# Kernel tuning notes

Measured on AMD Instinct MI355X. Metric: run time of the kernel, lower is better.

Reference implementation:

```python
import jax, jax.numpy as jnp
import numpy as np

N_NODES = 50000
N_EDGES = 800000
NFEAT, NHID, NCLASS = 256, 64, 2


def _deg_norm(idx, n_nodes, dtype):
    deg = jax.ops.segment_sum(jnp.ones(idx.shape[0], dtype=dtype), idx, num_segments=n_nodes)
    return jax.lax.rsqrt(jnp.maximum(deg, 1.0))


def gcn_layer(x, W, b, src, dst, n_nodes):
    # DGL GraphConv, norm='both': h = D_in^{-1/2} * Agg( D_out^{-1/2} * x ) W + b
    # weight applied before aggregation (in_feats >= out_feats path); math-equivalent.
    norm_src = _deg_norm(src, n_nodes, x.dtype)  # out-degree norm of source nodes
    norm_dst = _deg_norm(dst, n_nodes, x.dtype)  # in-degree norm of dest nodes
    h = (x * norm_src[:, None]) @ W              # [N, out]
    agg = jax.ops.segment_sum(h[src], dst, num_segments=n_nodes)  # gather + scatter-add
    return agg * norm_dst[:, None] + b


def setup_inputs() -> dict:
    key = jax.random.key(0)
    k1, k2, k3, k4, k5, k6, k7 = jax.random.split(key, 7)
    x = jax.random.normal(k1, (N_NODES, NFEAT), dtype=jnp.float32)
    src = jax.random.randint(k2, (N_EDGES,), 0, N_NODES, dtype=jnp.int64)
    dst = jax.random.randint(k3, (N_EDGES,), 0, N_NODES, dtype=jnp.int64)
    # Glorot-style init like DGL GraphConv
    W1 = jax.random.normal(k4, (NFEAT, NHID), dtype=jnp.float32) * (2.0 / (NFEAT + NHID)) ** 0.5
    b1 = jnp.zeros((NHID,), dtype=jnp.float32)
    W2 = jax.random.normal(k5, (NHID, NCLASS), dtype=jnp.float32) * (2.0 / (NHID + NCLASS)) ** 0.5
    b2 = jnp.zeros((NCLASS,), dtype=jnp.float32)
    return {"x": x, "src": src, "dst": dst, "W1": W1, "b1": b1, "W2": W2, "b2": b2}


def reference(x, src, dst, W1, b1, W2, b2):
    h = jax.nn.relu(gcn_layer(x, W1, b1, src, dst, N_NODES))
    # dropout=False -> p=0, no-op
    logits = gcn_layer(h, W2, b2, src, dst, N_NODES)
    return jax.nn.log_softmax(logits, axis=1)
```

## Files before the change

kernel.cpp:

```cpp
#include <hip/hip_runtime.h>
#include <math.h>

#define N_NODES 50000
#define N_EDGES 800000
#define NFEAT 256
#define NHID 64
#define NCLASS 2

#define DB 64
#define NDB 782
#define BCAP 1536
#define EPB 2048
#define NB_EDGE ((N_EDGES + EPB - 1) / EPB)

#define OFF_CURD 0
#define OFF_CURS 800
#define OFF_RB   1600
#define OFF_DEG  51600
#define OFF_NDST 101600
#define OFF_NSRC 151600
#define OFF_W1T  201600
#define OFF_DPK  209792
#define OFF_SV6  1410944
#define OFF_CSR  1711232
#define OFF_HB   2912384
#define OFF_H2   4512384

typedef __attribute__((ext_vector_type(8))) short bf16x8;
typedef __attribute__((ext_vector_type(8))) short short8;
typedef __attribute__((ext_vector_type(4))) float f32x4;

static __device__ __forceinline__ unsigned short f2bf(float f) {
    union { float f; unsigned int u; } v; v.f = f;
    return (unsigned short)((v.u + 0x8000u) >> 16);
}
static __device__ __forceinline__ unsigned int pk2bf(float f0, float f1) {
    union { float f; unsigned int u; } a, b; a.f = f0; b.f = f1;
    return __builtin_amdgcn_perm(b.u + 0x8000u, a.u + 0x8000u, 0x07060302u);
}
static __device__ __forceinline__ float bflo(unsigned int u) {
    union { unsigned int x; float f; } v; v.x = u << 16; return v.f;
}
static __device__ __forceinline__ float bfhi(unsigned int u) {
    union { unsigned int x; float f; } v; v.x = u & 0xffff0000u; return v.f;
}

__global__ __launch_bounds__(256) void w1cvt_kernel(const float* __restrict__ W1,
                                                    unsigned short* __restrict__ w1t) {
    int idx = blockIdx.x * 256 + threadIdx.x;
    if (idx < NFEAT * NHID) {
        int k = idx >> 6, n = idx & 63;
        w1t[n * NFEAT + k] = f2bf(W1[idx]);
    }
}

__global__ __launch_bounds__(256) void bscatter_kernel(const int* __restrict__ src,
                                                       const int* __restrict__ dst,
                                                       int* __restrict__ cur_d,
                                                       int* __restrict__ cur_s,
                                                       int* __restrict__ dpk,
                                                       unsigned char* __restrict__ sv6) {
    __shared__ int hd[NDB], bd[NDB], cd[NDB], hs[NDB], bs[NDB], cs[NDB];
    int t = threadIdx.x;
    for (int i = t; i < NDB; i += 256) { hd[i] = 0; cd[i] = 0; hs[i] = 0; cs[i] = 0; }
    __syncthreads();
    int base = blockIdx.x * EPB;
    int ls[8], ld[8];
#pragma unroll
    for (int i = 0; i < 8; ++i) {
        int e = base + t + i * 256;
        ls[i] = (e < N_EDGES) ? src[e] : -1;
        ld[i] = (e < N_EDGES) ? dst[e] : -1;
        if (ld[i] >= 0) {
            atomicAdd(&hd[ld[i] >> 6], 1);
            atomicAdd(&hs[ls[i] >> 6], 1);
        }
    }
    __syncthreads();
    for (int i = t; i < NDB; i += 256) {
        if (hd[i]) bd[i] = atomicAdd(&cur_d[i], hd[i]);
        if (hs[i]) bs[i] = atomicAdd(&cur_s[i], hs[i]);
    }
    __syncthreads();
#pragma unroll
    for (int i = 0; i < 8; ++i) {
        if (ld[i] >= 0) {
            int bin = ld[i] >> 6;
            int pos = bd[bin] + atomicAdd(&cd[bin], 1);
            dpk[bin * BCAP + pos] = (ls[i] << 6) | (ld[i] & 63);
            int sbin = ls[i] >> 6;
            int spos = bs[sbin] + atomicAdd(&cs[sbin], 1);
            sv6[sbin * BCAP + spos] = (unsigned char)(ls[i] & 63);
        }
    }
}

__global__ __launch_bounds__(256) void dfin_kernel(const int* __restrict__ cur_d,
                                                   const int* __restrict__ dpk,
                                                   int* __restrict__ row_beg,
                                                   int* __restrict__ degv,
                                                   float* __restrict__ norm_dst,
                                                   int* __restrict__ csr) {
    __shared__ int ebuf[BCAP];
    __shared__ int hist4[4 * 64], hist[64], seg[64], cur[64];
    int b = blockIdx.x, t = threadIdx.x;
    int cnt = cur_d[b];
    int base = b * BCAP;
    if (t < 64) { hist[t] = 0; cur[t] = 0; }
    hist4[t] = 0;
    for (int j = t; j < cnt; j += 256) ebuf[j] = dpk[base + j];
    __syncthreads();
    int sub = (t & 3) * 64;
    for (int j = t; j < cnt; j += 256) atomicAdd(&hist4[sub + (ebuf[j] & 63)], 1);
    __syncthreads();
    if (t < 64) {
        int v = hist4[t] + hist4[64 + t] + hist4[128 + t] + hist4[192 + t];
        hist[t] = v;
        seg[t] = v;
    }
    __syncthreads();
#pragma unroll
    for (int off = 1; off < 64; off <<= 1) {
        int xv = 0;
        if (t < 64 && t >= off) xv = seg[t - off];
        __syncthreads();
        if (t < 64) seg[t] += xv;
        __syncthreads();
    }
    if (t < 64) {
        int v = hist[t];
        int excl = seg[t] - v;
        int gid = b * 64 + t;
        if (gid < N_NODES) {
            row_beg[gid] = base + excl;
            degv[gid] = v;
            norm_dst[gid] = rsqrtf(fmaxf((float)v, 1.0f));
        }
        seg[t] = excl;
    }
    __syncthreads();
    for (int j = t; j < cnt; j += 256) {
        int p = ebuf[j];
        int dlow = p & 63;
        int pos = base + seg[dlow] + atomicAdd(&cur[dlow], 1);
        csr[pos] = ((unsigned)p) >> 6;
    }
}

__global__ __launch_bounds__(256) void sfin_kernel(const int* __restrict__ cur_s,
                                                   const unsigned char* __restrict__ sv6,
                                                   float* __restrict__ norm_src) {
    __shared__ int hist4[4 * 64];
    int b = blockIdx.x, t = threadIdx.x;
    hist4[t] = 0;
    __syncthreads();
    int cnt = cur_s[b];
    int base = b * BCAP;
    int sub = (t & 3) * 64;
    for (int j = t; j < cnt; j += 256) atomicAdd(&hist4[sub + sv6[base + j]], 1);
    __syncthreads();
    if (t < 64) {
        int gid = b * 64 + t;
        if (gid < N_NODES) {
            int v = hist4[t] + hist4[64 + t] + hist4[128 + t] + hist4[192 + t];
            norm_src[gid] = rsqrtf(fmaxf((float)v, 1.0f));
        }
    }
}

#define LDA 264
__global__ __launch_bounds__(256) void gemm1_kernel(const float* __restrict__ x,
                                                    const unsigned short* __restrict__ w1t,
                                                    const float* __restrict__ norm_src,
                                                    unsigned short* __restrict__ hb) {
    __shared__ unsigned short As[64][LDA];
    __shared__ unsigned short Bs[64][LDA];
    const int t = threadIdx.x;
    const int row0 = blockIdx.x * 64;
#pragma unroll
    for (int i = 0; i < 16; ++i) {
        int f = i * 256 + t;
        int r = f >> 6;
        int c4 = (f & 63) * 4;
        int grow = row0 + r;
        float4 av = make_float4(0.f, 0.f, 0.f, 0.f);
        if (grow < N_NODES) av = *(const float4*)(&x[(size_t)grow * NFEAT + c4]);
        uint2 o;
        o.x = pk2bf(av.x, av.y);
        o.y = pk2bf(av.z, av.w);
        *(uint2*)(&As[r][c4]) = o;
    }
#pragma unroll
    for (int i = 0; i < 8; ++i) {
        int c = i * 256 + t;
        int n = c >> 5;
        int k8 = (c & 31) * 8;
        *(short8*)(&Bs[n][k8]) = *(const short8*)(&w1t[n * NFEAT + k8]);
    }
    __syncthreads();
    const int w = t >> 6;
    const int l = t & 63;
    const int m = l & 15;
    const int kq = (l >> 4) * 8;
    f32x4 acc[4] = {{0.f, 0.f, 0.f, 0.f}, {0.f, 0.f, 0.f, 0.f},
                    {0.f, 0.f, 0.f, 0.f}, {0.f, 0.f, 0.f, 0.f}};
#pragma unroll
    for (int c8 = 0; c8 < 8; ++c8) {
        int k0 = c8 * 32 + kq;
        bf16x8 a = *(const bf16x8*)(&As[w * 16 + m][k0]);
#pragma unroll
        for (int ct = 0; ct < 4; ++ct) {
            bf16x8 b = *(const bf16x8*)(&Bs[ct * 16 + m][k0]);
            acc[ct] = __builtin_amdgcn_mfma_f32_16x16x32_bf16(a, b, acc[ct], 0, 0, 0);
        }
    }
    const int q = l >> 4;
#pragma unroll
    for (int reg = 0; reg < 4; ++reg) {
        int r = row0 + w * 16 + q * 4 + reg;
        if (r < N_NODES) {
            float ns = norm_src[r];
#pragma unroll
            for (int ct = 0; ct < 4; ++ct)
                hb[(size_t)r * NHID + ct * 16 + m] = f2bf(acc[ct][reg] * ns);
        }
    }
}

__global__ __launch_bounds__(256) void fused1_kernel(const int* __restrict__ row_beg,
                                                     const int* __restrict__ degv,
                                                     const int* __restrict__ csr,
                                                     const unsigned short* __restrict__ hb,
                                                     const float* __restrict__ norm_dst,
                                                     const float* __restrict__ norm_src,
                                                     const float* __restrict__ b1,
                                                     const float* __restrict__ W2,
                                                     float* __restrict__ h2) {
    int gtid = blockIdx.x * blockDim.x + threadIdx.x;
    int node = gtid >> 6;
    int lane = gtid & 63;
    if (node >= N_NODES) return;
    int e8 = lane >> 3, fg = lane & 7;
    int beg = row_beg[node];
    int end = beg + degv[node];
    float a0 = 0.f, a1 = 0.f, a2 = 0.f, a3 = 0.f, a4 = 0.f, a5 = 0.f, a6 = 0.f, a7 = 0.f;
    for (int j = beg; j < end; j += 16) {
        int j0 = j + e8, j1 = j0 + 8;
        uint4 u0 = make_uint4(0u, 0u, 0u, 0u), u1 = make_uint4(0u, 0u, 0u, 0u);
        if (j0 < end) u0 = *(const uint4*)(&hb[(size_t)csr[j0] * NHID + fg * 8]);
        if (j1 < end) u1 = *(const uint4*)(&hb[(size_t)csr[j1] * NHID + fg * 8]);
        a0 += bflo(u0.x) + bflo(u1.x);
        a1 += bfhi(u0.x) + bfhi(u1.x);
        a2 += bflo(u0.y) + bflo(u1.y);
        a3 += bfhi(u0.y) + bfhi(u1.y);
        a4 += bflo(u0.z) + bflo(u1.z);
        a5 += bfhi(u0.z) + bfhi(u1.z);
        a6 += bflo(u0.w) + bflo(u1.w);
        a7 += bfhi(u0.w) + bfhi(u1.w);
    }
#pragma unroll
    for (int off = 8; off <= 32; off <<= 1) {
        a0 += __shfl_xor(a0, off, 64);
        a1 += __shfl_xor(a1, off, 64);
        a2 += __shfl_xor(a2, off, 64);
        a3 += __shfl_xor(a3, off, 64);
        a4 += __shfl_xor(a4, off, 64);
        a5 += __shfl_xor(a5, off, 64);
        a6 += __shfl_xor(a6, off, 64);
        a7 += __shfl_xor(a7, off, 64);
    }
    float nd = norm_dst[node], ns = norm_src[node];
    float4 bv0 = *(const float4*)(&b1[fg * 8]);
    float4 bv1 = *(const float4*)(&b1[fg * 8 + 4]);
    float4 w0 = *(const float4*)(&W2[fg * 16 + 0]);
    float4 w1 = *(const float4*)(&W2[fg * 16 + 4]);
    float4 w2v = *(const float4*)(&W2[fg * 16 + 8]);
    float4 w3 = *(const float4*)(&W2[fg * 16 + 12]);
    float h0 = fmaxf(fmaf(a0, nd, bv0.x), 0.f) * ns;
    float h1 = fmaxf(fmaf(a1, nd, bv0.y), 0.f) * ns;
    float h2f = fmaxf(fmaf(a2, nd, bv0.z), 0.f) * ns;
    float h3 = fmaxf(fmaf(a3, nd, bv0.w), 0.f) * ns;
    float h4 = fmaxf(fmaf(a4, nd, bv1.x), 0.f) * ns;
    float h5 = fmaxf(fmaf(a5, nd, bv1.y), 0.f) * ns;
    float h6 = fmaxf(fmaf(a6, nd, bv1.z), 0.f) * ns;
    float h7 = fmaxf(fmaf(a7, nd, bv1.w), 0.f) * ns;
    float p0 = h0 * w0.x + h1 * w0.z + h2f * w1.x + h3 * w1.z +
               h4 * w2v.x + h5 * w2v.z + h6 * w3.x + h7 * w3.z;
    float p1 = h0 * w0.y + h1 * w0.w + h2f * w1.y + h3 * w1.w +
               h4 * w2v.y + h5 * w2v.w + h6 * w3.y + h7 * w3.w;
#pragma unroll
    for (int off = 1; off <= 4; off <<= 1) {
        p0 += __shfl_xor(p0, off, 64);
        p1 += __shfl_xor(p1, off, 64);
    }
    if (lane == 0) *(float2*)(&h2[node * 2]) = make_float2(p0, p1);
}

__global__ void fused2_kernel(const int* __restrict__ row_beg, const int* __restrict__ degv,
                              const int* __restrict__ csr, const float* __restrict__ h2,
                              const float* __restrict__ norm_dst, const float* __restrict__ b2,
                              float* __restrict__ out) {
    int n = blockIdx.x * blockDim.x + threadIdx.x;
    if (n >= N_NODES) return;
    int beg = row_beg[n], end = beg + degv[n];
    float s0 = 0.f, s1 = 0.f;
    for (int j = beg; j < end; ++j) {
        float2 v = *(const float2*)(&h2[csr[j] * 2]);
        s0 += v.x;
        s1 += v.y;
    }
    float nd = norm_dst[n];
    float l0 = fmaf(s0, nd, b2[0]);
    float l1 = fmaf(s1, nd, b2[1]);
    float m = fmaxf(l0, l1);
    float lse = m + logf(expf(l0 - m) + expf(l1 - m));
    *(float2*)(&out[n * 2]) = make_float2(l0 - lse, l1 - lse);
}

extern "C" void kernel_launch(void* const* d_in, const int* in_sizes, int n_in,
                              void* d_out, int out_size, void* d_ws, size_t ws_size,
                              hipStream_t stream) {
    const float* x  = (const float*)d_in[0];
    const int* src  = (const int*)d_in[1];
    const int* dst  = (const int*)d_in[2];
    const float* W1 = (const float*)d_in[3];
    const float* b1 = (const float*)d_in[4];
    const float* W2 = (const float*)d_in[5];
    const float* b2 = (const float*)d_in[6];
    float* out = (float*)d_out;
    float* ws  = (float*)d_ws;
    int*   wsi = (int*)d_ws;

    int*   cur_d    = wsi + OFF_CURD;
    int*   cur_s    = wsi + OFF_CURS;
    int*   row_beg  = wsi + OFF_RB;
    int*   degv     = wsi + OFF_DEG;
    float* norm_dst = ws + OFF_NDST;
    float* norm_src = ws + OFF_NSRC;
    unsigned short* w1t = (unsigned short*)(wsi + OFF_W1T);
    int*   dpk      = wsi + OFF_DPK;
    unsigned char* sv6 = (unsigned char*)(wsi + OFF_SV6);
    int*   csr      = wsi + OFF_CSR;
    unsigned short* hb = (unsigned short*)(wsi + OFF_HB);
    float* h2       = ws + OFF_H2;

    hipMemsetAsync(cur_d, 0, 1600 * sizeof(int), stream);
    w1cvt_kernel<<<(NFEAT * NHID + 255) / 256, 256, 0, stream>>>(W1, w1t);
    bscatter_kernel<<<NB_EDGE, 256, 0, stream>>>(src, dst, cur_d, cur_s, dpk, sv6);
    sfin_kernel<<<NDB, 256, 0, stream>>>(cur_s, sv6, norm_src);
    dfin_kernel<<<NDB, 256, 0, stream>>>(cur_d, dpk, row_beg, degv, norm_dst, csr);
    gemm1_kernel<<<(N_NODES + 63) / 64, 256, 0, stream>>>(x, w1t, norm_src, hb);
    {
        long long threads = (long long)N_NODES * 64;
        fused1_kernel<<<(int)((threads + 255) / 256), 256, 0, stream>>>(
            row_beg, degv, csr, hb, norm_dst, norm_src, b1, W2, h2);
    }
    fused2_kernel<<<(N_NODES + 255) / 256, 256, 0, stream>>>(row_beg, degv, csr, h2, norm_dst, b2, out);
}
```

Before: 191.1 us.

## Merge degree finalization and GEMM into one role-split kernel, move norm_src to gather

Folds the memset into the W1 conversion kernel, and merges the src-degree, dst-CSR and GEMM1 kernels into one launch whose blocks pick a role by blockIdx mod 3. To remove the GEMM's dependence on norm_src, the source normalization is now applied per edge in the aggregation loop, which loads norm_src[s] for every neighbour. The GEMM stages x in two K-halves to shrink LDS so it fits the shared union. This cuts launch count and serialization, at the cost of an extra scattered load per edge in the gather and a larger LDS footprint for every block.

```diff
diff --git a/kernel.cpp b/kernel.cpp
--- a/kernel.cpp
+++ b/kernel.cpp
@@ -45,10 +45,15 @@
     union { unsigned int x; float f; } v; v.x = u & 0xffff0000u; return v.f;
 }
 
-__global__ __launch_bounds__(256) void w1cvt_kernel(const float* __restrict__ W1,
-                                                    unsigned short* __restrict__ w1t) {
-    int idx = blockIdx.x * 256 + threadIdx.x;
-    if (idx < NFEAT * NHID) {
+#define INIT_N (1600 + NFEAT * NHID)
+__global__ __launch_bounds__(256) void init_kernel(const float* __restrict__ W1,
+                                                   int* __restrict__ cursors,
+                                                   unsigned short* __restrict__ w1t) {
+    int g = blockIdx.x * 256 + threadIdx.x;
+    if (g < 1600) {
+        cursors[g] = 0;
+    } else if (g < INIT_N) {
+        int idx = g - 1600;
         int k = idx >> 6, n = idx & 63;
         w1t[n * NFEAT + k] = f2bf(W1[idx]);
     }
@@ -95,134 +100,138 @@
     }
 }
 
-__global__ __launch_bounds__(256) void dfin_kernel(const int* __restrict__ cur_d,
-                                                   const int* __restrict__ dpk,
-                                                   int* __restrict__ row_beg,
-                                                   int* __restrict__ degv,
-                                                   float* __restrict__ norm_dst,
-                                                   int* __restrict__ csr) {
-    __shared__ int ebuf[BCAP];
-    __shared__ int hist4[4 * 64], hist[64], seg[64], cur[64];
-    int b = blockIdx.x, t = threadIdx.x;
-    int cnt = cur_d[b];
-    int base = b * BCAP;
-    if (t < 64) { hist[t] = 0; cur[t] = 0; }
-    hist4[t] = 0;
-    for (int j = t; j < cnt; j += 256) ebuf[j] = dpk[base + j];
-    __syncthreads();
-    int sub = (t & 3) * 64;
-    for (int j = t; j < cnt; j += 256) atomicAdd(&hist4[sub + (ebuf[j] & 63)], 1);
-    __syncthreads();
-    if (t < 64) {
-        int v = hist4[t] + hist4[64 + t] + hist4[128 + t] + hist4[192 + t];
-        hist[t] = v;
-        seg[t] = v;
-    }
-    __syncthreads();
-#pragma unroll
-    for (int off = 1; off < 64; off <<= 1) {
-        int xv = 0;
-        if (t < 64 && t >= off) xv = seg[t - off];
-        __syncthreads();
-        if (t < 64) seg[t] += xv;
-        __syncthreads();
-    }
-    if (t < 64) {
-        int v = hist[t];
-        int excl = seg[t] - v;
-        int gid = b * 64 + t;
-        if (gid < N_NODES) {
-            row_beg[gid] = base + excl;
-            degv[gid] = v;
-            norm_dst[gid] = rsqrtf(fmaxf((float)v, 1.0f));
-        }
-        seg[t] = excl;
-    }
-    __syncthreads();
-    for (int j = t; j < cnt; j += 256) {
-        int p = ebuf[j];
-        int dlow = p & 63;
-        int pos = base + seg[dlow] + atomicAdd(&cur[dlow], 1);
-        csr[pos] = ((unsigned)p) >> 6;
-    }
-}
-
-__global__ __launch_bounds__(256) void sfin_kernel(const int* __restrict__ cur_s,
-                                                   const unsigned char* __restrict__ sv6,
-                                                   float* __restrict__ norm_src) {
-    __shared__ int hist4[4 * 64];
-    int b = blockIdx.x, t = threadIdx.x;
-    hist4[t] = 0;
-    __syncthreads();
-    int cnt = cur_s[b];
-    int base = b * BCAP;
-    int sub = (t & 3) * 64;
-    for (int j = t; j < cnt; j += 256) atomicAdd(&hist4[sub + sv6[base + j]], 1);
-    __syncthreads();
-    if (t < 64) {
-        int gid = b * 64 + t;
-        if (gid < N_NODES) {
-            int v = hist4[t] + hist4[64 + t] + hist4[128 + t] + hist4[192 + t];
-            norm_src[gid] = rsqrtf(fmaxf((float)v, 1.0f));
-        }
-    }
-}
-
-#define LDA 264
-__global__ __launch_bounds__(256) void gemm1_kernel(const float* __restrict__ x,
-                                                    const unsigned short* __restrict__ w1t,
-                                                    const float* __restrict__ norm_src,
-                                                    unsigned short* __restrict__ hb) {
-    __shared__ unsigned short As[64][LDA];
-    __shared__ unsigned short Bs[64][LDA];
-    const int t = threadIdx.x;
-    const int row0 = blockIdx.x * 64;
-#pragma unroll
-    for (int i = 0; i < 16; ++i) {
-        int f = i * 256 + t;
-        int r = f >> 6;
-        int c4 = (f & 63) * 4;
-        int grow = row0 + r;
-        float4 av = make_float4(0.f, 0.f, 0.f, 0.f);
-        if (grow < N_NODES) av = *(const float4*)(&x[(size_t)grow * NFEAT + c4]);
-        uint2 o;
-        o.x = pk2bf(av.x, av.y);
-        o.y = pk2bf(av.z, av.w);
-        *(uint2*)(&As[r][c4]) = o;
-    }
-#pragma unroll
-    for (int i = 0; i < 8; ++i) {
-        int c = i * 256 + t;
-        int n = c >> 5;
-        int k8 = (c & 31) * 8;
-        *(short8*)(&Bs[n][k8]) = *(const short8*)(&w1t[n * NFEAT + k8]);
-    }
-    __syncthreads();
-    const int w = t >> 6;
-    const int l = t & 63;
-    const int m = l & 15;
-    const int kq = (l >> 4) * 8;
-    f32x4 acc[4] = {{0.f, 0.f, 0.f, 0.f}, {0.f, 0.f, 0.f, 0.f},
-                    {0.f, 0.f, 0.f, 0.f}, {0.f, 0.f, 0.f, 0.f}};
-#pragma unroll
-    for (int c8 = 0; c8 < 8; ++c8) {
-        int k0 = c8 * 32 + kq;
-        bf16x8 a = *(const bf16x8*)(&As[w * 16 + m][k0]);
-#pragma unroll
-        for (int ct = 0; ct < 4; ++ct) {
-            bf16x8 b = *(const bf16x8*)(&Bs[ct * 16 + m][k0]);
-            acc[ct] = __builtin_amdgcn_mfma_f32_16x16x32_bf16(a, b, acc[ct], 0, 0, 0);
-        }
-    }
-    const int q = l >> 4;
-#pragma unroll
-    for (int reg = 0; reg < 4; ++reg) {
-        int r = row0 + w * 16 + q * 4 + reg;
-        if (r < N_NODES) {
-            float ns = norm_src[r];
-#pragma unroll
-            for (int ct = 0; ct < 4; ++ct)
-                hb[(size_t)r * NHID + ct * 16 + m] = f2bf(acc[ct][reg] * ns);
+union MidShared {
+    struct { unsigned short As[64][136]; unsigned short Bs[64][264]; } g;
+    struct { int ebuf[BCAP]; int hist4[256]; int hist[64]; int seg[64]; int cur[64]; } d;
+    struct { int hist4[256]; } s;
+};
+__global__ __launch_bounds__(256) void mid_kernel(const int* __restrict__ cur_d,
+                                                  const int* __restrict__ cur_s,
+                                                  const int* __restrict__ dpk,
+                                                  const unsigned char* __restrict__ sv6,
+                                                  const float* __restrict__ x,
+                                                  const unsigned short* __restrict__ w1t,
+                                                  int* __restrict__ row_beg,
+                                                  int* __restrict__ degv,
+                                                  float* __restrict__ norm_dst,
+                                                  float* __restrict__ norm_src,
+                                                  int* __restrict__ csr,
+                                                  unsigned short* __restrict__ hb) {
+    __shared__ MidShared su;
+    int t = threadIdx.x;
+    int role = blockIdx.x % 3;
+    int b = blockIdx.x / 3;
+
+    if (role == 0) {
+        su.s.hist4[t] = 0;
+        __syncthreads();
+        int cnt = cur_s[b];
+        int base = b * BCAP;
+        int sub = (t & 3) * 64;
+        for (int j = t; j < cnt; j += 256) atomicAdd(&su.s.hist4[sub + sv6[base + j]], 1);
+        __syncthreads();
+        if (t < 64) {
+            int gid = b * 64 + t;
+            if (gid < N_NODES) {
+                int v = su.s.hist4[t] + su.s.hist4[64 + t] + su.s.hist4[128 + t] + su.s.hist4[192 + t];
+                norm_src[gid] = rsqrtf(fmaxf((float)v, 1.0f));
+            }
+        }
+    } else if (role == 1) {
+        int cnt = cur_d[b];
+        int base = b * BCAP;
+        if (t < 64) { su.d.hist[t] = 0; su.d.cur[t] = 0; }
+        su.d.hist4[t] = 0;
+        for (int j = t; j < cnt; j += 256) su.d.ebuf[j] = dpk[base + j];
+        __syncthreads();
+        int sub = (t & 3) * 64;
+        for (int j = t; j < cnt; j += 256) atomicAdd(&su.d.hist4[sub + (su.d.ebuf[j] & 63)], 1);
+        __syncthreads();
+        if (t < 64) {
+            int v = su.d.hist4[t] + su.d.hist4[64 + t] + su.d.hist4[128 + t] + su.d.hist4[192 + t];
+            su.d.hist[t] = v;
+            su.d.seg[t] = v;
+        }
+        __syncthreads();
+#pragma unroll
+        for (int off = 1; off < 64; off <<= 1) {
+            int xv = 0;
+            if (t < 64 && t >= off) xv = su.d.seg[t - off];
+            __syncthreads();
+            if (t < 64) su.d.seg[t] += xv;
+            __syncthreads();
+        }
+        if (t < 64) {
+            int v = su.d.hist[t];
+            int excl = su.d.seg[t] - v;
+            int gid = b * 64 + t;
+            if (gid < N_NODES) {
+                row_beg[gid] = base + excl;
+                degv[gid] = v;
+                norm_dst[gid] = rsqrtf(fmaxf((float)v, 1.0f));
+            }
+            su.d.seg[t] = excl;
+        }
+        __syncthreads();
+        for (int j = t; j < cnt; j += 256) {
+            int p = su.d.ebuf[j];
+            int dlow = p & 63;
+            int pos = base + su.d.seg[dlow] + atomicAdd(&su.d.cur[dlow], 1);
+            csr[pos] = ((unsigned)p) >> 6;
+        }
+    } else {
+        const int row0 = b * 64;
+#pragma unroll
+        for (int i = 0; i < 8; ++i) {
+            int c = i * 256 + t;
+            int n = c >> 5;
+            int k8 = (c & 31) * 8;
+            *(short8*)(&su.g.Bs[n][k8]) = *(const short8*)(&w1t[n * NFEAT + k8]);
+        }
+        const int w = t >> 6;
+        const int l = t & 63;
+        const int m = l & 15;
+        const int kq = (l >> 4) * 8;
+        const int q = l >> 4;
+        f32x4 acc[4] = {{0.f, 0.f, 0.f, 0.f}, {0.f, 0.f, 0.f, 0.f},
+                        {0.f, 0.f, 0.f, 0.f}, {0.f, 0.f, 0.f, 0.f}};
+#pragma unroll
+        for (int half = 0; half < 2; ++half) {
+            __syncthreads();
+#pragma unroll
+            for (int i = 0; i < 8; ++i) {
+                int f = i * 256 + t;
+                int r = f >> 5;
+                int c4 = (f & 31) * 4;
+                int grow = row0 + r;
+                float4 av = make_float4(0.f, 0.f, 0.f, 0.f);
+                if (grow < N_NODES)
+                    av = *(const float4*)(&x[(size_t)grow * NFEAT + half * 128 + c4]);
+                uint2 o;
+                o.x = pk2bf(av.x, av.y);
+                o.y = pk2bf(av.z, av.w);
+                *(uint2*)(&su.g.As[r][c4]) = o;
+            }
+            __syncthreads();
+#pragma unroll
+            for (int c8 = 0; c8 < 4; ++c8) {
+                int k0 = c8 * 32 + kq;
+                bf16x8 a = *(const bf16x8*)(&su.g.As[w * 16 + m][k0]);
+#pragma unroll
+                for (int ct = 0; ct < 4; ++ct) {
+                    bf16x8 bb = *(const bf16x8*)(&su.g.Bs[ct * 16 + m][half * 128 + k0]);
+                    acc[ct] = __builtin_amdgcn_mfma_f32_16x16x32_bf16(a, bb, acc[ct], 0, 0, 0);
+                }
+            }
+        }
+#pragma unroll
+        for (int reg = 0; reg < 4; ++reg) {
+            int r = row0 + w * 16 + q * 4 + reg;
+            if (r < N_NODES) {
+#pragma unroll
+                for (int ct = 0; ct < 4; ++ct)
+                    hb[(size_t)r * NHID + ct * 16 + m] = f2bf(acc[ct][reg]);
+            }
         }
     }
 }
@@ -247,16 +256,25 @@
     for (int j = beg; j < end; j += 16) {
         int j0 = j + e8, j1 = j0 + 8;
         uint4 u0 = make_uint4(0u, 0u, 0u, 0u), u1 = make_uint4(0u, 0u, 0u, 0u);
-        if (j0 < end) u0 = *(const uint4*)(&hb[(size_t)csr[j0] * NHID + fg * 8]);
-        if (j1 < end) u1 = *(const uint4*)(&hb[(size_t)csr[j1] * NHID + fg * 8]);
-        a0 += bflo(u0.x) + bflo(u1.x);
-        a1 += bfhi(u0.x) + bfhi(u1.x);
-        a2 += bflo(u0.y) + bflo(u1.y);
-        a3 += bfhi(u0.y) + bfhi(u1.y);
-        a4 += bflo(u0.z) + bflo(u1.z);
-        a5 += bfhi(u0.z) + bfhi(u1.z);
-        a6 += bflo(u0.w) + bflo(u1.w);
-        a7 += bfhi(u0.w) + bfhi(u1.w);
+        float ns0 = 0.f, ns1 = 0.f;
+        if (j0 < end) {
+            int s = csr[j0];
+            ns0 = norm_src[s];
+            u0 = *(const uint4*)(&hb[(size_t)s * NHID + fg * 8]);
+        }
+        if (j1 < end) {
+            int s = csr[j1];
+            ns1 = norm_src[s];
+            u1 = *(const uint4*)(&hb[(size_t)s * NHID + fg * 8]);
+        }
+        a0 = fmaf(ns0, bflo(u0.x), fmaf(ns1, bflo(u1.x), a0));
+        a1 = fmaf(ns0, bfhi(u0.x), fmaf(ns1, bfhi(u1.x), a1));
+        a2 = fmaf(ns0, bflo(u0.y), fmaf(ns1, bflo(u1.y), a2));
+        a3 = fmaf(ns0, bfhi(u0.y), fmaf(ns1, bfhi(u1.y), a3));
+        a4 = fmaf(ns0, bflo(u0.z), fmaf(ns1, bflo(u1.z), a4));
+        a5 = fmaf(ns0, bfhi(u0.z), fmaf(ns1, bfhi(u1.z), a5));
+        a6 = fmaf(ns0, bflo(u0.w), fmaf(ns1, bflo(u1.w), a6));
+        a7 = fmaf(ns0, bfhi(u0.w), fmaf(ns1, bfhi(u1.w), a7));
     }
 #pragma unroll
     for (int off = 8; off <= 32; off <<= 1) {
@@ -344,12 +362,10 @@
     unsigned short* hb = (unsigned short*)(wsi + OFF_HB);
     float* h2       = ws + OFF_H2;
 
-    hipMemsetAsync(cur_d, 0, 1600 * sizeof(int), stream);
-    w1cvt_kernel<<<(NFEAT * NHID + 255) / 256, 256, 0, stream>>>(W1, w1t);
+    init_kernel<<<(INIT_N + 255) / 256, 256, 0, stream>>>(W1, cur_d, w1t);
     bscatter_kernel<<<NB_EDGE, 256, 0, stream>>>(src, dst, cur_d, cur_s, dpk, sv6);
-    sfin_kernel<<<NDB, 256, 0, stream>>>(cur_s, sv6, norm_src);
-    dfin_kernel<<<NDB, 256, 0, stream>>>(cur_d, dpk, row_beg, degv, norm_dst, csr);
-    gemm1_kernel<<<(N_NODES + 63) / 64, 256, 0, stream>>>(x, w1t, norm_src, hb);
+    mid_kernel<<<NDB * 3, 256, 0, stream>>>(cur_d, cur_s, dpk, sv6, x, w1t,
+                                            row_beg, degv, norm_dst, norm_src, csr, hb);
     {
         long long threads = (long long)N_NODES * 64;
         fused1_kernel<<<(int)((threads + 255) / 256), 256, 0, stream>>>(
```

Result: faster. 184.3 us (-3.6%).
